# Kernel optimization log

Measured on AMD Instinct MI355X. Metric: run time of the kernel, lower is better.

The kernel has to match this reference:

```python
import jax, jax.numpy as jnp
import numpy as np

B, T, C = 4, 2048, 1024
H, D = 16, 64
SCALE = D ** -0.5


def setup_inputs() -> dict:
    key = jax.random.key(0)
    ks = jax.random.split(key, 5)
    s = 0.02
    return {
        "hidden_states": jax.random.normal(ks[0], (B, T, C), dtype=jnp.float32),
        "attention_mask": jnp.ones((B, T), dtype=jnp.int32),
        "Wq": jax.random.normal(ks[1], (C, H * D), dtype=jnp.float32) * s,
        "Wk": jax.random.normal(ks[2], (C, H * D), dtype=jnp.float32) * s,
        "Wv": jax.random.normal(ks[3], (C, H * D), dtype=jnp.float32) * s,
        "Wo": jax.random.normal(ks[4], (H * D, C), dtype=jnp.float32) * s,
        "bo": jnp.zeros((C,), dtype=jnp.float32),
    }


def reference(hidden_states, attention_mask, Wq, Wk, Wv, Wo, bo):
    b, t, _ = hidden_states.shape
    # projections -> (B, H, T, D)
    q = (hidden_states @ Wq).reshape(b, t, H, D).transpose(0, 2, 1, 3)
    k = (hidden_states @ Wk).reshape(b, t, H, D).transpose(0, 2, 1, 3)
    v = (hidden_states @ Wv).reshape(b, t, H, D).transpose(0, 2, 1, 3)
    # scores (B, H, Tq, Tk)
    scores = jnp.einsum("bhqd,bhkd->bhqk", q, k) * SCALE
    mask = attention_mask[:, None, None, :]  # (B,1,1,T), dim==2 branch
    scores = jnp.where(mask == 0, -jnp.inf, scores)
    probs = jax.nn.softmax(scores, axis=-1)
    out = jnp.einsum("bhqk,bhkd->bhqd", probs, v)
    out = out.transpose(0, 2, 1, 3).reshape(b, t, H * D)
    return out @ Wo + bo
```

## Files before the change

### kernel.cpp

```cpp
#include <hip/hip_runtime.h>
#include <hip/hip_bf16.h>

#define B_ 4
#define T_ 2048
#define C_ 1024
#define H_ 16
#define D_ 64
#define SCALE_ 0.125f
#define L2E 1.4426950408889634f
#define SE (SCALE_ * L2E)

typedef __attribute__((ext_vector_type(8))) short bf16x8;
typedef __attribute__((ext_vector_type(4))) float f32x4;

__device__ __forceinline__ unsigned short f2bf(float f) {
    union { float f; unsigned u; } v; v.f = f;
    unsigned r = v.u + 0x7fff + ((v.u >> 16) & 1);
    return (unsigned short)(r >> 16);
}

__device__ __forceinline__ unsigned pk2bf(float a, float b) {
    __hip_bfloat162 t = __float22bfloat162_rn(make_float2(a, b));
    union { __hip_bfloat162 h; unsigned u; } c; c.h = t;
    return c.u;
}

__device__ __forceinline__ void gl_lds16(const unsigned short* g, unsigned short* l) {
    __builtin_amdgcn_global_load_lds(
        (const __attribute__((address_space(1))) void*)g,
        (__attribute__((address_space(3))) void*)l,
        16, 0, 0);
}

__device__ __forceinline__ void bar_fence() {
    asm volatile("s_barrier" ::: "memory");
}

__global__ void cvtw_kernel(const float4* __restrict__ in, ushort4* __restrict__ out,
                            const float* __restrict__ Wq, const float* __restrict__ Wk,
                            const float* __restrict__ Wv, const float* __restrict__ Wo,
                            unsigned short* __restrict__ Wqkv_t, unsigned short* __restrict__ Wo_t) {
    __shared__ float tile[64][65];
    const int bid = blockIdx.x;
    const int t = threadIdx.x;
    if (bid < 8192) {
        int i = bid * 256 + t;
        float4 v = in[i];
        ushort4 o;
        o.x = f2bf(v.x); o.y = f2bf(v.y); o.z = f2bf(v.z); o.w = f2bf(v.w);
        out[i] = o;
        return;
    }
    const int wb = bid - 8192;
    const int mtx = wb >> 8;
    const float* W = (mtx == 0) ? Wq : (mtx == 1) ? Wk : (mtx == 2) ? Wv : Wo;
    unsigned short* Out = (mtx < 3) ? (Wqkv_t + (size_t)mtx * 1024 * 1024) : Wo_t;
    const int tl = wb & 255;
    const int tx = tl & 15, ty = tl >> 4;
    const int col = t & 63, rb = t >> 6;
#pragma unroll
    for (int rr = 0; rr < 16; ++rr) {
        int r = rb * 16 + rr;
        tile[r][col] = W[(size_t)(ty * 64 + r) * 1024 + tx * 64 + col];
    }
    __syncthreads();
#pragma unroll
    for (int rr = 0; rr < 16; ++rr) {
        int r = rb * 16 + rr;
        Out[(size_t)(tx * 64 + r) * 1024 + ty * 64 + col] = f2bf(tile[col][r]);
    }
}

__device__ __forceinline__ void qkv_stage_A(
    const unsigned short* __restrict__ A, unsigned short* Lsh,
    int slot, int kt, int m0, int tid, int w) {
#pragma unroll
    for (int i = 0; i < 2; ++i) {
        int idx = i * 512 + tid;
        int r = idx >> 3;
        int c2 = ((idx & 7) * 16) ^ ((r & 7) << 4);
        gl_lds16(A + (size_t)(m0 + r) * 1024 + kt * 64 + (c2 >> 1),
                 Lsh + slot * 8192 + (i * 512 + w * 64) * 8);
    }
}

__device__ __forceinline__ void qkv_stage_B(
    const unsigned short* __restrict__ Bt, unsigned short* Lsh,
    int slot, int kt, int n0, int tid, int w) {
#pragma unroll
    for (int i = 0; i < 4; ++i) {
        int idx = i * 512 + tid;
        int r = idx >> 3;
        int c2 = ((idx & 7) * 16) ^ ((r & 7) << 4);
        gl_lds16(Bt + (size_t)(n0 + r) * 1024 + kt * 64 + (c2 >> 1),
                 Lsh + 16384 + slot * 16384 + (i * 512 + w * 64) * 8);
    }
}

__global__ __launch_bounds__(512, 2) void gemm_qkv_kernel(
    const unsigned short* __restrict__ A, const unsigned short* __restrict__ Bt,
    unsigned short* __restrict__ Qg, unsigned short* __restrict__ Kf, unsigned short* __restrict__ Vf) {
    __shared__ __align__(16) unsigned short Lsh[49152];

    const int tid = threadIdx.x;
    const int w = tid >> 6, lane = tid & 63;
    const int quad = lane >> 4, l16 = lane & 15;
    const int wr = w >> 2, wc = w & 3;
    const int bid = blockIdx.x;
    const int swz = (bid & 7) * 96 + (bid >> 3);
    const int m0 = (swz & 63) * 128, n0 = (swz >> 6) * 256;

    const f32x4 fzero = {0.f, 0.f, 0.f, 0.f};
    f32x4 acc[4][4];
#pragma unroll
    for (int i = 0; i < 4; ++i)
#pragma unroll
        for (int j = 0; j < 4; ++j) acc[i][j] = fzero;

    qkv_stage_A(A, Lsh, 0, 0, m0, tid, w);
    qkv_stage_B(Bt, Lsh, 0, 0, n0, tid, w);
    asm volatile("s_waitcnt vmcnt(0)" ::: "memory");
    bar_fence();

#pragma unroll 1
    for (int kt = 0; kt < 16; ++kt) {
        const int slot = kt & 1;
        qkv_stage_A(A, Lsh, slot ^ 1, (kt + 1) & 15, m0, tid, w);
        qkv_stage_B(Bt, Lsh, slot ^ 1, (kt + 1) & 15, n0, tid, w);

#pragma unroll
        for (int ks = 0; ks < 2; ++ks) {
            bf16x8 a[4], b[4];
#pragma unroll
            for (int i = 0; i < 4; ++i) {
                int r = wr * 64 + i * 16 + l16;
                int cb = (ks * 64 + quad * 16) ^ ((r & 7) << 4);
                a[i] = *(const bf16x8*)(Lsh + slot * 8192 + r * 64 + (cb >> 1));
            }
#pragma unroll
            for (int j = 0; j < 4; ++j) {
                int r = wc * 64 + j * 16 + l16;
                int cb = (ks * 64 + quad * 16) ^ ((r & 7) << 4);
                b[j] = *(const bf16x8*)(Lsh + 16384 + slot * 16384 + r * 64 + (cb >> 1));
            }
            __builtin_amdgcn_s_setprio(1);
#pragma unroll
            for (int i = 0; i < 4; ++i)
#pragma unroll
                for (int j = 0; j < 4; ++j)
                    acc[i][j] = __builtin_amdgcn_mfma_f32_16x16x32_bf16(a[i], b[j], acc[i][j], 0, 0, 0);
            __builtin_amdgcn_s_setprio(0);
        }
        asm volatile("s_waitcnt vmcnt(0)" ::: "memory");
        bar_fence();
    }

#pragma unroll
    for (int j = 0; j < 4; ++j) {
        int gn = n0 + wc * 64 + j * 16 + l16;
        int tensor = gn >> 10;
        int nl = gn & 1023;
        int hh = nl >> 6, dd = nl & 63;
#pragma unroll
        for (int i = 0; i < 4; ++i) {
            int gmb = m0 + wr * 64 + i * 16 + quad * 4;
            int bb = gmb >> 11;
            size_t bhh = (size_t)(bb * 16 + hh);
            if (tensor == 0) {
#pragma unroll
                for (int r = 0; r < 4; ++r) {
                    int tt = (gmb + r) & 2047;
                    Qg[(bhh * 2048 + tt) * 64 + dd] = f2bf(acc[i][j][r] * SE);
                }
            } else if (tensor == 1) {
#pragma unroll
                for (int r = 0; r < 4; ++r) {
                    int tt = (gmb + r) & 2047;
                    Kf[bhh * 131072 + (size_t)(tt >> 4) * 1024 + (dd >> 5) * 512 +
                       (((dd >> 3) & 3) * 16 + (tt & 15)) * 8 + (dd & 7)] = f2bf(acc[i][j][r]);
                }
            } else {
                int tt = gmb & 2047;
                ushort4 v4;
                v4.x = f2bf(acc[i][j][0]); v4.y = f2bf(acc[i][j][1]);
                v4.z = f2bf(acc[i][j][2]); v4.w = f2bf(acc[i][j][3]);
                *(ushort4*)(Vf + bhh * 131072 + (size_t)(tt >> 5) * 2048 + (dd >> 4) * 512 +
                            (((tt >> 3) & 3) * 16 + (dd & 15)) * 8 + (tt & 7)) = v4;
            }
        }
    }
}

__device__ __forceinline__ void attn_step_staged(
    int k0, const unsigned short* Kc, const unsigned short* Vc,
    unsigned short* Kn, unsigned short* Vn, int kn0,
    const unsigned short* __restrict__ Kg, const unsigned short* __restrict__ Vg,
    unsigned short* Pw, const bf16x8 (&aq)[2][2], const bf16x8& vones,
    f32x4 (&po)[2][4], f32x4 (&pl)[2],
    const int* __restrict__ mrow, int w, int lane, int quad, int l16) {

    gl_lds16(Kg + (size_t)(kn0 >> 4) * 1024 + w * 512 + lane * 8, Kn + w * 512);
    gl_lds16(Vg + (size_t)(kn0 >> 5) * 2048 + w * 512 + lane * 8, Vn + w * 512);

    bf16x8 ka0[4], ka1[4];
#pragma unroll
    for (int kt = 0; kt < 4; ++kt) {
        ka0[kt] = *(const bf16x8*)(Kc + kt * 1024 + lane * 8);
        ka1[kt] = *(const bf16x8*)(Kc + kt * 1024 + 512 + lane * 8);
    }

    const f32x4 fzero = {0.f, 0.f, 0.f, 0.f};
    int mk = mrow[k0 + lane];
    bool allok = (__ballot(mk != 0) == 0xFFFFFFFFFFFFFFFFull);

    if (allok) {
#pragma unroll
        for (int kt = 0; kt < 4; ++kt) {
            int pidx = ((((kt & 1) << 1) | (quad >> 1)) * 16 + l16) * 8 + (quad & 1) * 4;
#pragma unroll
            for (int qi = 0; qi < 2; ++qi) {
                f32x4 st = __builtin_amdgcn_mfma_f32_16x16x32_bf16(ka0[kt], aq[qi][0], fzero, 0, 0, 0);
                st = __builtin_amdgcn_mfma_f32_16x16x32_bf16(ka1[kt], aq[qi][1], st, 0, 0, 0);
                float p0 = __builtin_amdgcn_exp2f(st[0]);
                float p1 = __builtin_amdgcn_exp2f(st[1]);
                float p2 = __builtin_amdgcn_exp2f(st[2]);
                float p3 = __builtin_amdgcn_exp2f(st[3]);
                uint2 pk; pk.x = pk2bf(p0, p1); pk.y = pk2bf(p2, p3);
                *(uint2*)(Pw + (qi * 2 + (kt >> 1)) * 512 + pidx) = pk;
            }
        }
    } else {
#pragma unroll
        for (int kt = 0; kt < 4; ++kt) {
            int4 mv = *(const int4*)(mrow + k0 + kt * 16 + quad * 4);
            float mb0 = mv.x ? 0.f : -1e30f;
            float mb1 = mv.y ? 0.f : -1e30f;
            float mb2 = mv.z ? 0.f : -1e30f;
            float mb3 = mv.w ? 0.f : -1e30f;
            int pidx = ((((kt & 1) << 1) | (quad >> 1)) * 16 + l16) * 8 + (quad & 1) * 4;
#pragma unroll
            for (int qi = 0; qi < 2; ++qi) {
                f32x4 st = __builtin_amdgcn_mfma_f32_16x16x32_bf16(ka0[kt], aq[qi][0], fzero, 0, 0, 0);
                st = __builtin_amdgcn_mfma_f32_16x16x32_bf16(ka1[kt], aq[qi][1], st, 0, 0, 0);
                float p0 = __builtin_amdgcn_exp2f(st[0] + mb0);
                float p1 = __builtin_amdgcn_exp2f(st[1] + mb1);
                float p2 = __builtin_amdgcn_exp2f(st[2] + mb2);
                float p3 = __builtin_amdgcn_exp2f(st[3] + mb3);
                uint2 pk; pk.x = pk2bf(p0, p1); pk.y = pk2bf(p2, p3);
                *(uint2*)(Pw + (qi * 2 + (kt >> 1)) * 512 + pidx) = pk;
            }
        }
    }

    bf16x8 bv[2][4];
#pragma unroll
    for (int c = 0; c < 2; ++c)
#pragma unroll
        for (int nd = 0; nd < 4; ++nd)
            bv[c][nd] = *(const bf16x8*)(Vc + c * 2048 + nd * 512 + lane * 8);

    asm volatile("s_waitcnt lgkmcnt(0)" ::: "memory");

#pragma unroll
    for (int c = 0; c < 2; ++c)
#pragma unroll
        for (int qi = 0; qi < 2; ++qi) {
            bf16x8 ap = *(const bf16x8*)(Pw + (qi * 2 + c) * 512 + lane * 8);
#pragma unroll
            for (int nd = 0; nd < 4; ++nd)
                po[qi][nd] = __builtin_amdgcn_mfma_f32_16x16x32_bf16(ap, bv[c][nd], po[qi][nd], 0, 0, 0);
            pl[qi] = __builtin_amdgcn_mfma_f32_16x16x32_bf16(ap, vones, pl[qi], 0, 0, 0);
        }
}

__global__ __launch_bounds__(512, 4) void attn_kernel(
    const unsigned short* __restrict__ Qg, const unsigned short* __restrict__ Kf,
    const unsigned short* __restrict__ Vf, const int* __restrict__ mask,
    unsigned short* __restrict__ AO) {
    __shared__ __align__(16) unsigned short KsA[4096], KsB[4096];
    __shared__ __align__(16) unsigned short VsA[4096], VsB[4096];
    __shared__ __align__(16) unsigned short Pbuf[8][2048];

    const int tid = threadIdx.x;
    const int w = tid >> 6, lane = tid & 63;
    const int quad = lane >> 4, l16 = lane & 15;
    const int bid = blockIdx.x;
    const int bh = (bid & 7) * 8 + ((bid >> 6) & 7);
    const int qt = (bid >> 3) & 7;
    const int b = bh >> 4, h = bh & 15;
    const size_t bh_td = (size_t)bh * (2048 * 64);
    const int q0w = qt * 256 + w * 32;

    bf16x8 aq[2][2];
#pragma unroll
    for (int qi = 0; qi < 2; ++qi)
#pragma unroll
        for (int hh = 0; hh < 2; ++hh)
            aq[qi][hh] = *(const bf16x8*)(Qg + bh_td + (size_t)(q0w + qi * 16 + l16) * 64 + hh * 32 + quad * 8);

    const unsigned short* Kg = Kf + bh_td;
    const unsigned short* Vg = Vf + bh_td;
    const int* mrow = mask + b * 2048;

    bf16x8 vones;
#pragma unroll
    for (int i = 0; i < 8; ++i) vones[i] = (short)0x3F80;

    const f32x4 fzero = {0.f, 0.f, 0.f, 0.f};
    f32x4 po[2][4];
    f32x4 pl[2];
#pragma unroll
    for (int qi = 0; qi < 2; ++qi) {
        pl[qi] = fzero;
#pragma unroll
        for (int nd = 0; nd < 4; ++nd) po[qi][nd] = fzero;
    }

    gl_lds16(Kg + w * 512 + lane * 8, KsA + w * 512);
    gl_lds16(Vg + w * 512 + lane * 8, VsA + w * 512);
    asm volatile("s_waitcnt vmcnt(0)" ::: "memory");
    __syncthreads();

#pragma unroll 1
    for (int k0 = 0; k0 < 2048; k0 += 128) {
        attn_step_staged(k0, KsA, VsA, KsB, VsB, k0 + 64,
                         Kg, Vg, Pbuf[w], aq, vones, po, pl, mrow, w, lane, quad, l16);
        asm volatile("s_waitcnt vmcnt(0)" ::: "memory");
        __syncthreads();
        attn_step_staged(k0 + 64, KsB, VsB, KsA, VsA, (k0 + 128) & 2047,
                         Kg, Vg, Pbuf[w], aq, vones, po, pl, mrow, w, lane, quad, l16);
        asm volatile("s_waitcnt vmcnt(0)" ::: "memory");
        __syncthreads();
    }

#pragma unroll
    for (int qi = 0; qi < 2; ++qi)
#pragma unroll
        for (int r = 0; r < 4; ++r) {
            float linv = __builtin_amdgcn_rcpf(pl[qi][r]);
            int q = q0w + qi * 16 + quad * 4 + r;
            size_t ob = (size_t)(b * 2048 + q) * 1024 + h * 64;
#pragma unroll
            for (int nd = 0; nd < 4; ++nd)
                AO[ob + nd * 16 + l16] = f2bf(po[qi][nd][r] * linv);
        }
}

__global__ __launch_bounds__(256) void gemm_out_kernel(
    const unsigned short* __restrict__ A, const unsigned short* __restrict__ Bt,
    const float* __restrict__ bo, float* __restrict__ out) {
    __shared__ __align__(16) unsigned short As[128 * 32];
    __shared__ __align__(16) unsigned short Bs[128 * 32];
    const int tid = threadIdx.x;
    const int w = tid >> 6, lane = tid & 63;
    const int quad = lane >> 4, l16 = lane & 15;
    const int m0 = blockIdx.y * 128, n0 = blockIdx.x * 128;
    const int mw = (w >> 1) * 64, nw = (w & 1) * 64;
    const int K = 1024;
    const int srow = lane >> 2;
    const int scol = (lane & 3) * 8;

    const f32x4 fzero = {0.f, 0.f, 0.f, 0.f};
    f32x4 acc[4][4];
#pragma unroll
    for (int i = 0; i < 4; ++i)
#pragma unroll
        for (int j = 0; j < 4; ++j) acc[i][j] = fzero;

    for (int k0 = 0; k0 < K; k0 += 32) {
        gl_lds16(A + (size_t)(m0 + w * 32 + srow) * K + k0 + scol,       As + (w * 32) * 32);
        gl_lds16(A + (size_t)(m0 + w * 32 + 16 + srow) * K + k0 + scol,  As + (w * 32 + 16) * 32);
        gl_lds16(Bt + (size_t)(n0 + w * 32 + srow) * K + k0 + scol,      Bs + (w * 32) * 32);
        gl_lds16(Bt + (size_t)(n0 + w * 32 + 16 + srow) * K + k0 + scol, Bs + (w * 32 + 16) * 32);
        __syncthreads();
        bf16x8 a[4], b[4];
#pragma unroll
        for (int i = 0; i < 4; ++i)
            a[i] = *(const bf16x8*)(As + (mw + i * 16 + l16) * 32 + quad * 8);
#pragma unroll
        for (int j = 0; j < 4; ++j)
            b[j] = *(const bf16x8*)(Bs + (nw + j * 16 + l16) * 32 + quad * 8);
#pragma unroll
        for (int i = 0; i < 4; ++i)
#pragma unroll
            for (int j = 0; j < 4; ++j)
                acc[i][j] = __builtin_amdgcn_mfma_f32_16x16x32_bf16(a[i], b[j], acc[i][j], 0, 0, 0);
        __syncthreads();
    }

#pragma unroll
    for (int j = 0; j < 4; ++j) {
        int gn = n0 + nw + j * 16 + l16;
        float bias = bo[gn];
#pragma unroll
        for (int i = 0; i < 4; ++i) {
            int gmb = m0 + mw + i * 16 + quad * 4;
#pragma unroll
            for (int r = 0; r < 4; ++r)
                out[(size_t)(gmb + r) * 1024 + gn] = acc[i][j][r] + bias;
        }
    }
}

extern "C" void kernel_launch(void* const* d_in, const int* in_sizes, int n_in,
                              void* d_out, int out_size, void* d_ws, size_t ws_size,
                              hipStream_t stream) {
    const float* hs  = (const float*)d_in[0];
    const int* mask  = (const int*)d_in[1];
    const float* Wq  = (const float*)d_in[2];
    const float* Wk  = (const float*)d_in[3];
    const float* Wv  = (const float*)d_in[4];
    const float* Wo  = (const float*)d_in[5];
    const float* bo  = (const float*)d_in[6];
    float* out = (float*)d_out;

    char* ws = (char*)d_ws;
    unsigned short* hs_bf = (unsigned short*)(ws);
    unsigned short* wqkv  = (unsigned short*)(ws + 16777216);
    unsigned short* wo_t  = (unsigned short*)(ws + 23068672);
    unsigned short* Qg    = (unsigned short*)(ws + 25165824);
    unsigned short* Kf    = (unsigned short*)(ws + 41943040);
    unsigned short* Vf    = (unsigned short*)(ws + 58720256);
    unsigned short* AO    = (unsigned short*)(ws + 75497472);

    cvtw_kernel<<<9216, 256, 0, stream>>>((const float4*)hs, (ushort4*)hs_bf,
                                          Wq, Wk, Wv, Wo, wqkv, wo_t);
    gemm_qkv_kernel<<<768, 512, 0, stream>>>(hs_bf, wqkv, Qg, Kf, Vf);
    attn_kernel<<<512, 512, 0, stream>>>(Qg, Kf, Vf, mask, AO);
    gemm_out_kernel<<<dim3(8, 64), 256, 0, stream>>>(AO, wo_t, bo, out);
}
```

Before: 270.5 us.

## Reuse pipelined 128x256 swizzled GEMM loop for output projection

Factors the QKV GEMM main loop into a shared helper and rewrites the output projection kernel to use it. The output GEMM moves from 128x128 tiles with a single unpipelined LDS buffer and BK=32 to 128x256 tiles with double-buffered, XOR-swizzled LDS staging, BK=64 and 512 threads. This aims to cut per-iteration barrier stalls and LDS bank conflicts and to improve data reuse. It leaves fewer blocks (256) to fill the device, which can hurt load balance.

```diff
diff --git a/kernel.cpp b/kernel.cpp
--- a/kernel.cpp
+++ b/kernel.cpp
@@ -97,6 +97,49 @@
     }
 }
 
+__device__ __forceinline__ void gemm_128x256_loop(
+    const unsigned short* __restrict__ A, const unsigned short* __restrict__ Bt,
+    unsigned short* Lsh, f32x4 (&acc)[4][4],
+    int m0, int n0, int tid, int w, int wr, int wc, int quad, int l16) {
+    qkv_stage_A(A, Lsh, 0, 0, m0, tid, w);
+    qkv_stage_B(Bt, Lsh, 0, 0, n0, tid, w);
+    asm volatile("s_waitcnt vmcnt(0)" ::: "memory");
+    bar_fence();
+
+#pragma unroll 1
+    for (int kt = 0; kt < 16; ++kt) {
+        const int slot = kt & 1;
+        qkv_stage_A(A, Lsh, slot ^ 1, (kt + 1) & 15, m0, tid, w);
+        qkv_stage_B(Bt, Lsh, slot ^ 1, (kt + 1) & 15, n0, tid, w);
+
+#pragma unroll
+        for (int ks = 0; ks < 2; ++ks) {
+            bf16x8 a[4], b[4];
+#pragma unroll
+            for (int i = 0; i < 4; ++i) {
+                int r = wr * 64 + i * 16 + l16;
+                int cb = (ks * 64 + quad * 16) ^ ((r & 7) << 4);
+                a[i] = *(const bf16x8*)(Lsh + slot * 8192 + r * 64 + (cb >> 1));
+            }
+#pragma unroll
+            for (int j = 0; j < 4; ++j) {
+                int r = wc * 64 + j * 16 + l16;
+                int cb = (ks * 64 + quad * 16) ^ ((r & 7) << 4);
+                b[j] = *(const bf16x8*)(Lsh + 16384 + slot * 16384 + r * 64 + (cb >> 1));
+            }
+            __builtin_amdgcn_s_setprio(1);
+#pragma unroll
+            for (int i = 0; i < 4; ++i)
+#pragma unroll
+                for (int j = 0; j < 4; ++j)
+                    acc[i][j] = __builtin_amdgcn_mfma_f32_16x16x32_bf16(a[i], b[j], acc[i][j], 0, 0, 0);
+            __builtin_amdgcn_s_setprio(0);
+        }
+        asm volatile("s_waitcnt vmcnt(0)" ::: "memory");
+        bar_fence();
+    }
+}
+
 __global__ __launch_bounds__(512, 2) void gemm_qkv_kernel(
     const unsigned short* __restrict__ A, const unsigned short* __restrict__ Bt,
     unsigned short* __restrict__ Qg, unsigned short* __restrict__ Kf, unsigned short* __restrict__ Vf) {
@@ -117,43 +160,7 @@
 #pragma unroll
         for (int j = 0; j < 4; ++j) acc[i][j] = fzero;
 
-    qkv_stage_A(A, Lsh, 0, 0, m0, tid, w);
-    qkv_stage_B(Bt, Lsh, 0, 0, n0, tid, w);
-    asm volatile("s_waitcnt vmcnt(0)" ::: "memory");
-    bar_fence();
-
-#pragma unroll 1
-    for (int kt = 0; kt < 16; ++kt) {
-        const int slot = kt & 1;
-        qkv_stage_A(A, Lsh, slot ^ 1, (kt + 1) & 15, m0, tid, w);
-        qkv_stage_B(Bt, Lsh, slot ^ 1, (kt + 1) & 15, n0, tid, w);
-
-#pragma unroll
-        for (int ks = 0; ks < 2; ++ks) {
-            bf16x8 a[4], b[4];
-#pragma unroll
-            for (int i = 0; i < 4; ++i) {
-                int r = wr * 64 + i * 16 + l16;
-                int cb = (ks * 64 + quad * 16) ^ ((r & 7) << 4);
-                a[i] = *(const bf16x8*)(Lsh + slot * 8192 + r * 64 + (cb >> 1));
-            }
-#pragma unroll
-            for (int j = 0; j < 4; ++j) {
-                int r = wc * 64 + j * 16 + l16;
-                int cb = (ks * 64 + quad * 16) ^ ((r & 7) << 4);
-                b[j] = *(const bf16x8*)(Lsh + 16384 + slot * 16384 + r * 64 + (cb >> 1));
-            }
-            __builtin_amdgcn_s_setprio(1);
-#pragma unroll
-            for (int i = 0; i < 4; ++i)
-#pragma unroll
-                for (int j = 0; j < 4; ++j)
-                    acc[i][j] = __builtin_amdgcn_mfma_f32_16x16x32_bf16(a[i], b[j], acc[i][j], 0, 0, 0);
-            __builtin_amdgcn_s_setprio(0);
-        }
-        asm volatile("s_waitcnt vmcnt(0)" ::: "memory");
-        bar_fence();
-    }
+    gemm_128x256_loop(A, Bt, Lsh, acc, m0, n0, tid, w, wr, wc, quad, l16);
 
 #pragma unroll
     for (int j = 0; j < 4; ++j) {
@@ -191,6 +198,42 @@
     }
 }
 
+__global__ __launch_bounds__(512, 2) void gemm_out_kernel(
+    const unsigned short* __restrict__ A, const unsigned short* __restrict__ Bt,
+    const float* __restrict__ bo, float* __restrict__ out) {
+    __shared__ __align__(16) unsigned short Lsh[49152];
+
+    const int tid = threadIdx.x;
+    const int w = tid >> 6, lane = tid & 63;
+    const int quad = lane >> 4, l16 = lane & 15;
+    const int wr = w >> 2, wc = w & 3;
+    const int bid = blockIdx.x;
+    const int swz = (bid & 7) * 32 + (bid >> 3);
+    const int m0 = (swz & 63) * 128, n0 = (swz >> 6) * 256;
+
+    const f32x4 fzero = {0.f, 0.f, 0.f, 0.f};
+    f32x4 acc[4][4];
+#pragma unroll
+    for (int i = 0; i < 4; ++i)
+#pragma unroll
+        for (int j = 0; j < 4; ++j) acc[i][j] = fzero;
+
+    gemm_128x256_loop(A, Bt, Lsh, acc, m0, n0, tid, w, wr, wc, quad, l16);
+
+#pragma unroll
+    for (int j = 0; j < 4; ++j) {
+        int gn = n0 + wc * 64 + j * 16 + l16;
+        float bias = bo[gn];
+#pragma unroll
+        for (int i = 0; i < 4; ++i) {
+            int gmb = m0 + wr * 64 + i * 16 + quad * 4;
+#pragma unroll
+            for (int r = 0; r < 4; ++r)
+                out[(size_t)(gmb + r) * 1024 + gn] = acc[i][j][r] + bias;
+        }
+    }
+}
+
 __device__ __forceinline__ void attn_step_staged(
     int k0, const unsigned short* Kc, const unsigned short* Vc,
     unsigned short* Kn, unsigned short* Vn, int kn0,
@@ -344,62 +387,6 @@
             for (int nd = 0; nd < 4; ++nd)
                 AO[ob + nd * 16 + l16] = f2bf(po[qi][nd][r] * linv);
         }
-}
-
-__global__ __launch_bounds__(256) void gemm_out_kernel(
-    const unsigned short* __restrict__ A, const unsigned short* __restrict__ Bt,
-    const float* __restrict__ bo, float* __restrict__ out) {
-    __shared__ __align__(16) unsigned short As[128 * 32];
-    __shared__ __align__(16) unsigned short Bs[128 * 32];
-    const int tid = threadIdx.x;
-    const int w = tid >> 6, lane = tid & 63;
-    const int quad = lane >> 4, l16 = lane & 15;
-    const int m0 = blockIdx.y * 128, n0 = blockIdx.x * 128;
-    const int mw = (w >> 1) * 64, nw = (w & 1) * 64;
-    const int K = 1024;
-    const int srow = lane >> 2;
-    const int scol = (lane & 3) * 8;
-
-    const f32x4 fzero = {0.f, 0.f, 0.f, 0.f};
-    f32x4 acc[4][4];
-#pragma unroll
-    for (int i = 0; i < 4; ++i)
-#pragma unroll
-        for (int j = 0; j < 4; ++j) acc[i][j] = fzero;
-
-    for (int k0 = 0; k0 < K; k0 += 32) {
-        gl_lds16(A + (size_t)(m0 + w * 32 + srow) * K + k0 + scol,       As + (w * 32) * 32);
-        gl_lds16(A + (size_t)(m0 + w * 32 + 16 + srow) * K + k0 + scol,  As + (w * 32 + 16) * 32);
-        gl_lds16(Bt + (size_t)(n0 + w * 32 + srow) * K + k0 + scol,      Bs + (w * 32) * 32);
-        gl_lds16(Bt + (size_t)(n0 + w * 32 + 16 + srow) * K + k0 + scol, Bs + (w * 32 + 16) * 32);
-        __syncthreads();
-        bf16x8 a[4], b[4];
-#pragma unroll
-        for (int i = 0; i < 4; ++i)
-            a[i] = *(const bf16x8*)(As + (mw + i * 16 + l16) * 32 + quad * 8);
-#pragma unroll
-        for (int j = 0; j < 4; ++j)
-            b[j] = *(const bf16x8*)(Bs + (nw + j * 16 + l16) * 32 + quad * 8);
-#pragma unroll
-        for (int i = 0; i < 4; ++i)
-#pragma unroll
-            for (int j = 0; j < 4; ++j)
-                acc[i][j] = __builtin_amdgcn_mfma_f32_16x16x32_bf16(a[i], b[j], acc[i][j], 0, 0, 0);
-        __syncthreads();
-    }
-
-#pragma unroll
-    for (int j = 0; j < 4; ++j) {
-        int gn = n0 + nw + j * 16 + l16;
-        float bias = bo[gn];
-#pragma unroll
-        for (int i = 0; i < 4; ++i) {
-            int gmb = m0 + mw + i * 16 + quad * 4;
-#pragma unroll
-            for (int r = 0; r < 4; ++r)
-                out[(size_t)(gmb + r) * 1024 + gn] = acc[i][j][r] + bias;
-        }
-    }
 }
 
 extern "C" void kernel_launch(void* const* d_in, const int* in_sizes, int n_in,
@@ -427,5 +414,5 @@
                                           Wq, Wk, Wv, Wo, wqkv, wo_t);
     gemm_qkv_kernel<<<768, 512, 0, stream>>>(hs_bf, wqkv, Qg, Kf, Vf);
     attn_kernel<<<512, 512, 0, stream>>>(Qg, Kf, Vf, mask, AO);
-    gemm_out_kernel<<<dim3(8, 64), 256, 0, stream>>>(AO, wo_t, bo, out);
-}
+    gemm_out_kernel<<<256, 512, 0, stream>>>(AO, wo_t, bo, out);
+}
```

Result: no change. 269.9 us (-0.2%).
